# Optimization experiments

Measured on AMD Instinct MI355X. Metric: run time of the kernel, lower is better.

The kernel has to match this reference:

```python
import jax, jax.numpy as jnp
import numpy as np

B, T, U, QS, MS = 64, 2048, 512, 512, 512

def setup_inputs() -> dict:
    key = jax.random.key(0)
    k1, k2, k3, k4, k5 = jax.random.split(key, 5)
    query = jax.random.normal(k1, (B, QS), dtype=jnp.float32)
    keys = jax.random.normal(k2, (B, T, MS), dtype=jnp.float32)
    # torch nn.Linear weights: [out, in], no bias
    Wq = jax.random.normal(k3, (U, QS), dtype=jnp.float32) * (1.0 / np.sqrt(QS))
    Wm = jax.random.normal(k4, (U, MS), dtype=jnp.float32) * (1.0 / np.sqrt(MS))
    Wa = jax.random.normal(k5, (1, U), dtype=jnp.float32) * (1.0 / np.sqrt(U))
    return {"query": query, "keys": keys, "Wq": Wq, "Wm": Wm, "Wa": Wa}

def reference(query, keys, Wq, Wm, Wa):
    # processed_query: [B, U]
    pq = jnp.einsum('bq,uq->bu', query, Wq)
    # values: [B, T, U]
    vals = jnp.einsum('btm,um->btu', keys, Wm)
    # alignment score: [B, T]
    score = jnp.einsum('btu,u->bt', jnp.tanh(pq[:, None, :] + vals), Wa[0])
    weight = jax.nn.softmax(score, axis=-1)            # [B, T]
    total_context = jnp.einsum('bt,btm->bm', weight, keys)  # [B, MS]
    return (total_context, score)
```

## Files before the change

### kernel.cpp

```cpp
#include <hip/hip_runtime.h>
#include <cstdint>
#include <cstddef>

#define Bn 64
#define Tn 2048
#define Un 512
#define QSn 512
#define MSn 512
#define TCH 64
#define NCH 32

using f32x16 = __attribute__((ext_vector_type(16))) float;
using bf16x8 = __attribute__((ext_vector_type(8))) short;

__device__ __forceinline__ unsigned short f2bf(float x) {
    unsigned int u = __float_as_uint(x);
    u += 0x7FFFu + ((u >> 16) & 1u);
    return (unsigned short)(u >> 16);
}

__device__ __forceinline__ unsigned int pk2bf(float lo, float hi) {
    unsigned int r;
    asm("v_cvt_pk_bf16_f32 %0, %1, %2" : "=v"(r) : "v"(lo), "v"(hi));
    return r;
}

__device__ __forceinline__ bf16x8 cvt8(float4 a, float4 b) {
    union { unsigned int u[4]; bf16x8 v; } r;
    r.u[0] = pk2bf(a.x, a.y);
    r.u[1] = pk2bf(a.z, a.w);
    r.u[2] = pk2bf(b.x, b.y);
    r.u[3] = pk2bf(b.z, b.w);
    return r.v;
}

__device__ __forceinline__ float tanh_fast(float x) {
    float e = exp2f(x * 2.885390043258667f);
    return 1.f - 2.f * __builtin_amdgcn_rcpf(e + 1.f);
}

#define GLOAD(G, L) __builtin_amdgcn_global_load_lds( \
    (const __attribute__((address_space(1))) void*)(G), \
    (__attribute__((address_space(3))) void*)(L), 16, 0, 0)

#define PIPE_BAR(N) do { \
    asm volatile("s_waitcnt vmcnt(" #N ") lgkmcnt(0)" ::: "memory"); \
    __builtin_amdgcn_s_barrier(); \
    __builtin_amdgcn_sched_barrier(0); } while (0)

__global__ __launch_bounds__(256) void cvt_kernel(const float* __restrict__ src,
                                                  unsigned short* __restrict__ dst) {
    int i = blockIdx.x * 256 + threadIdx.x;
    float4 v = *(const float4*)(src + (size_t)i * 4);
    ushort4 h = { f2bf(v.x), f2bf(v.y), f2bf(v.z), f2bf(v.w) };
    *(ushort4*)&dst[(size_t)i * 4] = h;
}

__global__ __launch_bounds__(128) void pq_kernel(const float* __restrict__ query,
                                                 const float* __restrict__ Wq,
                                                 float* __restrict__ pq) {
    __shared__ float ql[QSn];
    const int b = blockIdx.x;
    const int quad = blockIdx.y;
    const int tid = threadIdx.x;
    for (int i = tid; i < QSn; i += 128) ql[i] = query[(size_t)b * QSn + i];
    __syncthreads();
    const int u = quad * 128 + tid;
    const float* w = Wq + (size_t)u * QSn;
    float a0 = 0.f, a1 = 0.f;
    #pragma unroll 4
    for (int k = 0; k < QSn; k += 8) {
        float4 w0 = *(const float4*)(w + k);
        float4 w1 = *(const float4*)(w + k + 4);
        float4 q0 = *(const float4*)(ql + k);
        float4 q1 = *(const float4*)(ql + k + 4);
        a0 += w0.x * q0.x + w0.y * q0.y + w0.z * q0.z + w0.w * q0.w;
        a1 += w1.x * q1.x + w1.y * q1.y + w1.z * q1.z + w1.w * q1.w;
    }
    pq[(size_t)b * Un + u] = a0 + a1;
}

__global__ __launch_bounds__(256, 2) void fused_kernel(const float* __restrict__ keys,
                                                       const unsigned short* __restrict__ WmB,
                                                       const float* __restrict__ pq,
                                                       const float* __restrict__ Wa,
                                                       float* __restrict__ score_out,
                                                       float* __restrict__ pm,
                                                       float* __restrict__ pl,
                                                       float* __restrict__ pctx) {
    __shared__ __align__(16) unsigned short Ah[2][TCH * 64];
    __shared__ __align__(16) unsigned short Bh[2][128 * 64];
    __shared__ float sc_lds[2][TCH];
    __shared__ float stot[TCH];
    __shared__ float wexp[TCH];

    const int tid = threadIdx.x;
    const int lane = tid & 63;
    const int w = tid >> 6;
    const int wm = w >> 1;
    const int wn = w & 1;
    const int lc = lane & 31;
    const int l5 = lane >> 5;
    const int b = blockIdx.y;
    const int chunk = blockIdx.x;
    const int t0 = chunk * TCH;

    const int ar = tid >> 2;
    const int g0 = (tid & 3) * 2;
    const float* gA = keys + ((size_t)b * Tn + t0 + ar) * MSn + g0 * 8;
    const int wofA0 = ar * 64 + ((g0 ^ (ar & 7)) * 8);
    const int wofA1 = ar * 64 + (((g0 + 1) ^ (ar & 7)) * 8);

    const int srow = lane >> 3;
    const int sco = (((lane & 7) ^ srow) << 3);
    const unsigned short* gBw = WmB + ((size_t)(w * 32 + srow)) * MSn + sco;
    char* bD0 = (char*)&Bh[0][0] + w * 4096;
    char* bD1 = (char*)&Bh[1][0] + w * 4096;

    f32x16 acc[4][2];
    #pragma unroll
    for (int uh = 0; uh < 4; ++uh)
        #pragma unroll
        for (int nf = 0; nf < 2; ++nf)
            #pragma unroll
            for (int r = 0; r < 16; ++r) acc[uh][nf][r] = 0.f;

    float4 sA0, sA1, sA2, sA3;

    #define GB(UH, KT, DST) do { \
        const unsigned short* p_ = gBw + (size_t)(UH) * 128 * MSn + (KT) * 64; \
        GLOAD(p_, (DST)); \
        GLOAD(p_ + (size_t)8 * MSn, (DST) + 1024); \
        GLOAD(p_ + (size_t)16 * MSn, (DST) + 2048); \
        GLOAD(p_ + (size_t)24 * MSn, (DST) + 3072); } while (0)

    #define MFMA_PHASE(UH, BUF) do { \
        _Pragma("unroll") \
        for (int ks = 0; ks < 4; ++ks) { \
            bf16x8 bfr0, bfr1; \
            { int ru = wn * 64 + lc; \
              bfr0 = *(const bf16x8*)&(BUF)[ru * 64 + (((ks * 2 + l5) ^ (ru & 7)) * 8)]; } \
            { int ru = wn * 64 + 32 + lc; \
              bfr1 = *(const bf16x8*)&(BUF)[ru * 64 + (((ks * 2 + l5) ^ (ru & 7)) * 8)]; } \
            acc[UH][0] = __builtin_amdgcn_mfma_f32_32x32x16_bf16(afr[ks], bfr0, acc[UH][0], 0, 0, 0); \
            acc[UH][1] = __builtin_amdgcn_mfma_f32_32x32x16_bf16(afr[ks], bfr1, acc[UH][1], 0, 0, 0); \
        } } while (0)

    GB(0, 0, bD0);
    __builtin_amdgcn_sched_barrier(0);
    sA0 = *(const float4*)(gA);
    sA1 = *(const float4*)(gA + 4);
    sA2 = *(const float4*)(gA + 8);
    sA3 = *(const float4*)(gA + 12);
    *(bf16x8*)&Ah[0][wofA0] = cvt8(sA0, sA1);
    *(bf16x8*)&Ah[0][wofA1] = cvt8(sA2, sA3);
    PIPE_BAR(0);

    #pragma unroll
    for (int kt = 0; kt < 8; ++kt) {
        const int cur = kt & 1;
        const unsigned short* lA = &Ah[cur][0];
        bf16x8 afr[4];

        GB(1, kt, bD1);
        __builtin_amdgcn_sched_barrier(0);
        #pragma unroll
        for (int ks = 0; ks < 4; ++ks) {
            int r = wm * 32 + lc;
            afr[ks] = *(const bf16x8*)&lA[r * 64 + (((ks * 2 + l5) ^ (r & 7)) * 8)];
        }
        MFMA_PHASE(0, Bh[0]);
        PIPE_BAR(0);

        GB(2, kt, bD0);
        __builtin_amdgcn_sched_barrier(0);
        if (kt < 7) {
            const float* g = gA + (kt + 1) * 64;
            sA0 = *(const float4*)(g);
            sA1 = *(const float4*)(g + 4);
            sA2 = *(const float4*)(g + 8);
            sA3 = *(const float4*)(g + 12);
        }
        __builtin_amdgcn_sched_barrier(0);
        MFMA_PHASE(1, Bh[1]);
        if (kt < 7) { PIPE_BAR(4); } else { PIPE_BAR(0); }

        GB(3, kt, bD1);
        __builtin_amdgcn_sched_barrier(0);
        MFMA_PHASE(2, Bh[0]);
        PIPE_BAR(0);

        if (kt < 7) { GB(0, kt + 1, bD0); }
        __builtin_amdgcn_sched_barrier(0);
        MFMA_PHASE(3, Bh[1]);
        if (kt < 7) {
            *(bf16x8*)&Ah[cur ^ 1][wofA0] = cvt8(sA0, sA1);
            *(bf16x8*)&Ah[cur ^ 1][wofA1] = cvt8(sA2, sA3);
        }
        PIPE_BAR(0);
    }
    #undef GB
    #undef MFMA_PHASE

    float pqv[4][2], wav[4][2];
    #pragma unroll
    for (int uh = 0; uh < 4; ++uh)
        #pragma unroll
        for (int nf = 0; nf < 2; ++nf) {
            int u = uh * 128 + wn * 64 + nf * 32 + lc;
            pqv[uh][nf] = pq[(size_t)b * Un + u];
            wav[uh][nf] = Wa[u];
        }
    #pragma unroll
    for (int r = 0; r < 16; ++r) {
        float s = 0.f;
        #pragma unroll
        for (int uh = 0; uh < 4; ++uh)
            #pragma unroll
            for (int nf = 0; nf < 2; ++nf)
                s += tanh_fast(acc[uh][nf][r] + pqv[uh][nf]) * wav[uh][nf];
        s += __shfl_xor(s, 16);
        s += __shfl_xor(s, 8);
        s += __shfl_xor(s, 4);
        s += __shfl_xor(s, 2);
        s += __shfl_xor(s, 1);
        if (lc == 0)
            sc_lds[wn][wm * 32 + (r & 3) + 8 * (r >> 2) + 4 * l5] = s;
    }
    __syncthreads();
    if (tid < TCH) {
        float v = sc_lds[0][tid] + sc_lds[1][tid];
        stot[tid] = v;
        score_out[(size_t)b * Tn + t0 + tid] = v;
    }
    __syncthreads();

    if (tid < 64) {
        float v = stot[tid];
        float mx = v;
        #pragma unroll
        for (int off = 32; off; off >>= 1) mx = fmaxf(mx, __shfl_xor(mx, off));
        float e = __expf(v - mx);
        wexp[tid] = e;
        float sum = e;
        #pragma unroll
        for (int off = 32; off; off >>= 1) sum += __shfl_xor(sum, off);
        if (tid == 0) {
            pm[b * NCH + chunk] = mx;
            pl[b * NCH + chunk] = sum;
        }
    }
    __syncthreads();

    const int c0 = tid * 2;
    const float* kp = keys + ((size_t)b * Tn + t0) * MSn + c0;
    float cx = 0.f, cy = 0.f;
    #pragma unroll 8
    for (int t = 0; t < TCH; ++t) {
        float2 kv = *(const float2*)(kp + (size_t)t * MSn);
        float wt = wexp[t];
        cx += wt * kv.x;
        cy += wt * kv.y;
    }
    float2 cacc = { cx, cy };
    *(float2*)&pctx[((size_t)(b * NCH + chunk)) * MSn + c0] = cacc;
}

__global__ __launch_bounds__(512) void merge_kernel(const float* __restrict__ pm,
                                                    const float* __restrict__ pl,
                                                    const float* __restrict__ pctx,
                                                    float* __restrict__ ctx) {
    __shared__ float sm[NCH], sl[NCH];
    const int b = blockIdx.x, tid = threadIdx.x;
    if (tid < NCH) {
        sm[tid] = pm[b * NCH + tid];
        sl[tid] = pl[b * NCH + tid];
    }
    __syncthreads();
    float M = -1e30f;
    #pragma unroll
    for (int c = 0; c < NCH; ++c) M = fmaxf(M, sm[c]);
    float L = 0.f;
    #pragma unroll
    for (int c = 0; c < NCH; ++c) L += sl[c] * __expf(sm[c] - M);
    const float inv = 1.f / L;
    float acc = 0.f;
    #pragma unroll
    for (int c = 0; c < NCH; ++c)
        acc += __expf(sm[c] - M) * pctx[((size_t)(b * NCH + c)) * MSn + tid];
    ctx[(size_t)b * MSn + tid] = acc * inv;
}

extern "C" void kernel_launch(void* const* d_in, const int* in_sizes, int n_in,
                              void* d_out, int out_size, void* d_ws, size_t ws_size,
                              hipStream_t stream) {
    const float* query = (const float*)d_in[0];
    const float* keys  = (const float*)d_in[1];
    const float* Wq    = (const float*)d_in[2];
    const float* Wm    = (const float*)d_in[3];
    const float* Wa    = (const float*)d_in[4];

    float* ctx_out   = (float*)d_out;
    float* score_out = (float*)d_out + (size_t)Bn * MSn;

    char* ws = (char*)d_ws;
    float* ws_pq   = (float*)(ws);
    unsigned short* ws_wmbf = (unsigned short*)(ws + 131072);
    float* ws_pm   = (float*)(ws + 655360);
    float* ws_pl   = (float*)(ws + 663552);
    float* ws_pctx = (float*)(ws + 671744);

    cvt_kernel<<<(Un * MSn / 4) / 256, 256, 0, stream>>>(Wm, ws_wmbf);
    pq_kernel<<<dim3(Bn, 4), 128, 0, stream>>>(query, Wq, ws_pq);
    fused_kernel<<<dim3(NCH, Bn), 256, 0, stream>>>(keys, ws_wmbf, ws_pq, Wa,
                                                    score_out, ws_pm, ws_pl, ws_pctx);
    merge_kernel<<<Bn, 512, 0, stream>>>(ws_pm, ws_pl, ws_pctx, ctx_out);
}
```

Measured before the change: 179.5 us.

## Give each wave its own Wm slice with double-buffered K=32 pipeline

The fused GEMM changes from a 2x2 wave grid that cycles through four 128-column weight phases per K-step to a layout where each wave owns a fixed 128-column slice of Wm across all 64 rows, with K tiles halved to 32 and 16 iterations. Each wave streams its own B tile into a private double buffer, and the A tile is shared, so barriers drop from four per K-step to one. This is meant to cut synchronisation and keep MFMAs fed more steadily. The cost is that each wave reloads A fragments for all 64 rows, the score reduction now sums across four waves, and the per-wave B buffers use more LDS.

```diff
diff --git a/kernel.cpp b/kernel.cpp
--- a/kernel.cpp
+++ b/kernel.cpp
@@ -9,6 +9,7 @@
 #define MSn 512
 #define TCH 64
 #define NCH 32
+#define NKT 16
 
 using f32x16 = __attribute__((ext_vector_type(16))) float;
 using bf16x8 = __attribute__((ext_vector_type(8))) short;
@@ -42,11 +43,6 @@
 #define GLOAD(G, L) __builtin_amdgcn_global_load_lds( \
     (const __attribute__((address_space(1))) void*)(G), \
     (__attribute__((address_space(3))) void*)(L), 16, 0, 0)
-
-#define PIPE_BAR(N) do { \
-    asm volatile("s_waitcnt vmcnt(" #N ") lgkmcnt(0)" ::: "memory"); \
-    __builtin_amdgcn_s_barrier(); \
-    __builtin_amdgcn_sched_barrier(0); } while (0)
 
 __global__ __launch_bounds__(256) void cvt_kernel(const float* __restrict__ src,
                                                   unsigned short* __restrict__ dst) {
@@ -88,148 +84,137 @@
                                                        float* __restrict__ pm,
                                                        float* __restrict__ pl,
                                                        float* __restrict__ pctx) {
-    __shared__ __align__(16) unsigned short Ah[2][TCH * 64];
-    __shared__ __align__(16) unsigned short Bh[2][128 * 64];
-    __shared__ float sc_lds[2][TCH];
+    __shared__ __align__(16) unsigned short Ah[2][TCH * 32];
+    __shared__ __align__(16) unsigned short Bh[4][2][128 * 32];
+    __shared__ float sc_lds[4][TCH];
     __shared__ float stot[TCH];
     __shared__ float wexp[TCH];
 
     const int tid = threadIdx.x;
     const int lane = tid & 63;
     const int w = tid >> 6;
-    const int wm = w >> 1;
-    const int wn = w & 1;
     const int lc = lane & 31;
     const int l5 = lane >> 5;
     const int b = blockIdx.y;
     const int chunk = blockIdx.x;
     const int t0 = chunk * TCH;
 
-    const int ar = tid >> 2;
-    const int g0 = (tid & 3) * 2;
-    const float* gA = keys + ((size_t)b * Tn + t0 + ar) * MSn + g0 * 8;
-    const int wofA0 = ar * 64 + ((g0 ^ (ar & 7)) * 8);
-    const int wofA1 = ar * 64 + (((g0 + 1) ^ (ar & 7)) * 8);
-
-    const int srow = lane >> 3;
-    const int sco = (((lane & 7) ^ srow) << 3);
-    const unsigned short* gBw = WmB + ((size_t)(w * 32 + srow)) * MSn + sco;
-    char* bD0 = (char*)&Bh[0][0] + w * 4096;
-    char* bD1 = (char*)&Bh[1][0] + w * 4096;
-
-    f32x16 acc[4][2];
-    #pragma unroll
-    for (int uh = 0; uh < 4; ++uh)
+    const int arow = tid >> 2;
+    const int akg = tid & 3;
+    const int awof = (tid >> 3) * 64 +
+                     ((((akg << 1) | (arow & 1)) ^ ((tid >> 3) & 7)) * 8);
+    const float* gA = keys + ((size_t)b * Tn + t0 + arow) * MSn + akg * 8;
+
+    const int bg = (lane & 7) ^ ((lane >> 3) & 7);
+    const size_t bloff = (size_t)(((lane >> 3) << 1) | (bg & 1)) * MSn + (bg >> 1) * 8;
+    const unsigned short* gBw = WmB + (size_t)(w * 128) * MSn + bloff;
+    char* bD = (char*)&Bh[w][0][0];
+
+    f32x16 acc[2][4];
+    #pragma unroll
+    for (int mf = 0; mf < 2; ++mf)
         #pragma unroll
-        for (int nf = 0; nf < 2; ++nf)
+        for (int nf = 0; nf < 4; ++nf)
             #pragma unroll
-            for (int r = 0; r < 16; ++r) acc[uh][nf][r] = 0.f;
-
-    float4 sA0, sA1, sA2, sA3;
-
-    #define GB(UH, KT, DST) do { \
-        const unsigned short* p_ = gBw + (size_t)(UH) * 128 * MSn + (KT) * 64; \
-        GLOAD(p_, (DST)); \
-        GLOAD(p_ + (size_t)8 * MSn, (DST) + 1024); \
-        GLOAD(p_ + (size_t)16 * MSn, (DST) + 2048); \
-        GLOAD(p_ + (size_t)24 * MSn, (DST) + 3072); } while (0)
-
-    #define MFMA_PHASE(UH, BUF) do { \
-        _Pragma("unroll") \
-        for (int ks = 0; ks < 4; ++ks) { \
-            bf16x8 bfr0, bfr1; \
-            { int ru = wn * 64 + lc; \
-              bfr0 = *(const bf16x8*)&(BUF)[ru * 64 + (((ks * 2 + l5) ^ (ru & 7)) * 8)]; } \
-            { int ru = wn * 64 + 32 + lc; \
-              bfr1 = *(const bf16x8*)&(BUF)[ru * 64 + (((ks * 2 + l5) ^ (ru & 7)) * 8)]; } \
-            acc[UH][0] = __builtin_amdgcn_mfma_f32_32x32x16_bf16(afr[ks], bfr0, acc[UH][0], 0, 0, 0); \
-            acc[UH][1] = __builtin_amdgcn_mfma_f32_32x32x16_bf16(afr[ks], bfr1, acc[UH][1], 0, 0, 0); \
-        } } while (0)
-
-    GB(0, 0, bD0);
+            for (int r = 0; r < 16; ++r) acc[mf][nf][r] = 0.f;
+
+    float4 a0, a1;
+
+    a0 = *(const float4*)(gA);
+    a1 = *(const float4*)(gA + 4);
     __builtin_amdgcn_sched_barrier(0);
-    sA0 = *(const float4*)(gA);
-    sA1 = *(const float4*)(gA + 4);
-    sA2 = *(const float4*)(gA + 8);
-    sA3 = *(const float4*)(gA + 12);
-    *(bf16x8*)&Ah[0][wofA0] = cvt8(sA0, sA1);
-    *(bf16x8*)&Ah[0][wofA1] = cvt8(sA2, sA3);
-    PIPE_BAR(0);
-
-    #pragma unroll
-    for (int kt = 0; kt < 8; ++kt) {
+    #pragma unroll
+    for (int j = 0; j < 8; ++j)
+        GLOAD(gBw + (size_t)j * 16 * MSn, bD + j * 1024);
+    __builtin_amdgcn_sched_barrier(0);
+    asm volatile("s_waitcnt vmcnt(8)" ::: "memory");
+    __builtin_amdgcn_sched_barrier(0);
+    *(bf16x8*)&Ah[0][awof] = cvt8(a0, a1);
+    asm volatile("s_waitcnt lgkmcnt(0)" ::: "memory");
+    __builtin_amdgcn_s_barrier();
+    __builtin_amdgcn_sched_barrier(0);
+
+    #pragma unroll
+    for (int kt = 0; kt < NKT; ++kt) {
         const int cur = kt & 1;
-        const unsigned short* lA = &Ah[cur][0];
-        bf16x8 afr[4];
-
-        GB(1, kt, bD1);
+
+        if (kt < NKT - 1) {
+            const float* g = gA + (kt + 1) * 32;
+            a0 = *(const float4*)(g);
+            a1 = *(const float4*)(g + 4);
+            __builtin_amdgcn_sched_barrier(0);
+            const unsigned short* gb = gBw + (kt + 1) * 32;
+            char* bdn = bD + (cur ^ 1) * 8192;
+            #pragma unroll
+            for (int j = 0; j < 8; ++j)
+                GLOAD(gb + (size_t)j * 16 * MSn, bdn + j * 1024);
+            __builtin_amdgcn_sched_barrier(0);
+            asm volatile("s_waitcnt vmcnt(10)" ::: "memory");
+        } else {
+            asm volatile("s_waitcnt vmcnt(0)" ::: "memory");
+        }
         __builtin_amdgcn_sched_barrier(0);
+
+        {
+            const unsigned short* lA = &Ah[cur][0];
+            const unsigned short* lB = &Bh[w][cur][0];
+            #pragma unroll
+            for (int ks = 0; ks < 2; ++ks) {
+                bf16x8 af[2];
+                #pragma unroll
+                for (int mf = 0; mf < 2; ++mf) {
+                    int r = mf * 32 + lc;
+                    int gp = (((ks * 2 + l5) << 1) | (r & 1)) ^ ((r >> 1) & 7);
+                    af[mf] = *(const bf16x8*)&lA[(r >> 1) * 64 + gp * 8];
+                }
+                #pragma unroll
+                for (int nf = 0; nf < 4; ++nf) {
+                    int ru = nf * 32 + lc;
+                    int gp = (((ks * 2 + l5) << 1) | (ru & 1)) ^ ((ru >> 1) & 7);
+                    bf16x8 bfr = *(const bf16x8*)&lB[(ru >> 1) * 64 + gp * 8];
+                    acc[0][nf] = __builtin_amdgcn_mfma_f32_32x32x16_bf16(af[0], bfr, acc[0][nf], 0, 0, 0);
+                    acc[1][nf] = __builtin_amdgcn_mfma_f32_32x32x16_bf16(af[1], bfr, acc[1][nf], 0, 0, 0);
+                }
+            }
+        }
+
+        if (kt < NKT - 1) {
+            asm volatile("s_waitcnt vmcnt(8)" ::: "memory");
+            __builtin_amdgcn_sched_barrier(0);
+            *(bf16x8*)&Ah[cur ^ 1][awof] = cvt8(a0, a1);
+            asm volatile("s_waitcnt lgkmcnt(0)" ::: "memory");
+            __builtin_amdgcn_s_barrier();
+            __builtin_amdgcn_sched_barrier(0);
+        }
+    }
+
+    float pqv[4], wav[4];
+    #pragma unroll
+    for (int nf = 0; nf < 4; ++nf) {
+        int u = w * 128 + nf * 32 + lc;
+        pqv[nf] = pq[(size_t)b * Un + u];
+        wav[nf] = Wa[u];
+    }
+    #pragma unroll
+    for (int mf = 0; mf < 2; ++mf) {
         #pragma unroll
-        for (int ks = 0; ks < 4; ++ks) {
-            int r = wm * 32 + lc;
-            afr[ks] = *(const bf16x8*)&lA[r * 64 + (((ks * 2 + l5) ^ (r & 7)) * 8)];
-        }
-        MFMA_PHASE(0, Bh[0]);
-        PIPE_BAR(0);
-
-        GB(2, kt, bD0);
-        __builtin_amdgcn_sched_barrier(0);
-        if (kt < 7) {
-            const float* g = gA + (kt + 1) * 64;
-            sA0 = *(const float4*)(g);
-            sA1 = *(const float4*)(g + 4);
-            sA2 = *(const float4*)(g + 8);
-            sA3 = *(const float4*)(g + 12);
-        }
-        __builtin_amdgcn_sched_barrier(0);
-        MFMA_PHASE(1, Bh[1]);
-        if (kt < 7) { PIPE_BAR(4); } else { PIPE_BAR(0); }
-
-        GB(3, kt, bD1);
-        __builtin_amdgcn_sched_barrier(0);
-        MFMA_PHASE(2, Bh[0]);
-        PIPE_BAR(0);
-
-        if (kt < 7) { GB(0, kt + 1, bD0); }
-        __builtin_amdgcn_sched_barrier(0);
-        MFMA_PHASE(3, Bh[1]);
-        if (kt < 7) {
-            *(bf16x8*)&Ah[cur ^ 1][wofA0] = cvt8(sA0, sA1);
-            *(bf16x8*)&Ah[cur ^ 1][wofA1] = cvt8(sA2, sA3);
-        }
-        PIPE_BAR(0);
-    }
-    #undef GB
-    #undef MFMA_PHASE
-
-    float pqv[4][2], wav[4][2];
-    #pragma unroll
-    for (int uh = 0; uh < 4; ++uh)
-        #pragma unroll
-        for (int nf = 0; nf < 2; ++nf) {
-            int u = uh * 128 + wn * 64 + nf * 32 + lc;
-            pqv[uh][nf] = pq[(size_t)b * Un + u];
-            wav[uh][nf] = Wa[u];
-        }
-    #pragma unroll
-    for (int r = 0; r < 16; ++r) {
-        float s = 0.f;
-        #pragma unroll
-        for (int uh = 0; uh < 4; ++uh)
+        for (int r = 0; r < 16; ++r) {
+            float s = 0.f;
             #pragma unroll
-            for (int nf = 0; nf < 2; ++nf)
-                s += tanh_fast(acc[uh][nf][r] + pqv[uh][nf]) * wav[uh][nf];
-        s += __shfl_xor(s, 16);
-        s += __shfl_xor(s, 8);
-        s += __shfl_xor(s, 4);
-        s += __shfl_xor(s, 2);
-        s += __shfl_xor(s, 1);
-        if (lc == 0)
-            sc_lds[wn][wm * 32 + (r & 3) + 8 * (r >> 2) + 4 * l5] = s;
+            for (int nf = 0; nf < 4; ++nf)
+                s += tanh_fast(acc[mf][nf][r] + pqv[nf]) * wav[nf];
+            s += __shfl_xor(s, 16);
+            s += __shfl_xor(s, 8);
+            s += __shfl_xor(s, 4);
+            s += __shfl_xor(s, 2);
+            s += __shfl_xor(s, 1);
+            if (lc == 0)
+                sc_lds[w][mf * 32 + (r & 3) + 8 * (r >> 2) + 4 * l5] = s;
+        }
     }
     __syncthreads();
     if (tid < TCH) {
-        float v = sc_lds[0][tid] + sc_lds[1][tid];
+        float v = (sc_lds[0][tid] + sc_lds[1][tid]) + (sc_lds[2][tid] + sc_lds[3][tid]);
         stot[tid] = v;
         score_out[(size_t)b * Tn + t0 + tid] = v;
     }
```

Result: slower. 187.2 us (+4.3%).
